# Kernel optimization log

Measured on AMD Instinct MI355X. Metric: run time of the kernel, lower is better.

The kernel has to match this reference:

```python
import jax, jax.numpy as jnp
import numpy as np

N_NODES, N_EDGES, CH, FEAT = 20000, 320000, 256, 118


def setup_inputs() -> dict:
    key = jax.random.key(0)
    ks = jax.random.split(key, 8)
    x = jax.random.uniform(ks[0], (N_NODES, FEAT), dtype=jnp.float32)
    edge_index = jax.random.randint(ks[1], (2, N_EDGES), 0, N_NODES, dtype=jnp.int64)
    s = 0.05
    W_embed = jax.random.normal(ks[2], (FEAT, CH), dtype=jnp.float32) * s
    b_embed = jnp.zeros((CH,), jnp.float32)
    W1 = jax.random.normal(ks[3], (CH, CH), dtype=jnp.float32) * s
    b1 = jnp.zeros((CH,), jnp.float32)
    W2 = jax.random.normal(ks[4], (CH, CH), dtype=jnp.float32) * s
    b2 = jnp.zeros((CH,), jnp.float32)
    return {"x": x, "edge_index": edge_index, "W_embed": W_embed, "b_embed": b_embed,
            "W1": W1, "b1": b1, "W2": W2, "b2": b2}


def reference(x, edge_index, W_embed, b_embed, W1, b1, W2, b2):
    n = x.shape[0]
    # node embedding: Linear(118 -> C)
    h = x @ W_embed + b_embed  # [N, C]
    src, dst = edge_index[0], edge_index[1]
    # message: gather x_j per edge, dense1 + exact GELU (dropout = identity in eval)
    msg = jax.nn.gelu(h[src] @ W1 + b1, approximate=False)  # [E, C]
    # mean aggregation into destination nodes
    agg = jax.ops.segment_sum(msg, dst, num_segments=n)  # [N, C]
    cnt = jax.ops.segment_sum(jnp.ones((msg.shape[0],), msg.dtype), dst, num_segments=n)
    agg = agg / jnp.maximum(cnt, 1.0)[:, None]
    # update: dense2 + exact GELU
    out = jax.nn.gelu(agg @ W2 + b2, approximate=False)  # [N, C]
    # final mean over channel dim
    return out.mean(axis=1)  # [N]
```

## Files before the change

### kernel.cpp

```cpp
#include <hip/hip_runtime.h>
#include <math.h>

#define N_NODES 20000
#define N_EDGES 320000
#define CH      256
#define FEAT    118
#define CAP     48

typedef float    f32x4 __attribute__((ext_vector_type(4)));
typedef short    s16x8 __attribute__((ext_vector_type(8)));
typedef _Float16 f16x4 __attribute__((ext_vector_type(4)));
typedef _Float16 f16x8 __attribute__((ext_vector_type(8)));
typedef unsigned short u16;

union Frag  { s16x8 v; u16 u[8]; };
union FragH { f16x8 v; _Float16 h[8]; };

__device__ __forceinline__ float gelu_exact(float x) {
    return 0.5f * x * (1.0f + erff(x * 0.70710678118654752f));
}
__device__ __forceinline__ u16 f2bf(float f) {
    unsigned u = __float_as_uint(f);
    u = (u + 0x7FFFu + ((u >> 16) & 1u)) >> 16;
    return (u16)u;
}
__device__ __forceinline__ float bf2f(u16 h) { return __uint_as_float(((unsigned)h) << 16); }

__global__ __launch_bounds__(256) void prep(const float* __restrict__ x,
                                            const int* __restrict__ ei,
                                            const float* __restrict__ We,
                                            const float* __restrict__ be,
                                            const float* __restrict__ W1,
                                            const float* __restrict__ b1,
                                            const float* __restrict__ W2,
                                            u16* __restrict__ xh, u16* __restrict__ xl,
                                            int* __restrict__ cnt, int* __restrict__ bins,
                                            _Float16* __restrict__ w2h, _Float16* __restrict__ w2l,
                                            u16* __restrict__ wch, u16* __restrict__ wcl,
                                            float* __restrict__ bc) {
    const int b = blockIdx.x, tid = threadIdx.x;
    if (b < 1250) {
        __shared__ float xs[16][132];
        {
            int r = tid >> 4, ci = tid & 15;
            const float* xrow = x + (size_t)(b * 16 + r) * FEAT;
            #pragma unroll
            for (int it = 0; it < 8; it++) {
                int col = ci + it * 16;
                xs[r][col] = (col < FEAT) ? xrow[col] : 0.0f;
            }
        }
        __syncthreads();
        int lane = tid & 63, ks = tid >> 6;
        int row = lane & 15, k0 = ks * 32 + (lane >> 4) * 8;
        Frag hi, lo;
        #pragma unroll
        for (int j = 0; j < 8; j++) {
            float v = xs[row][k0 + j];
            u16 h = f2bf(v);
            hi.u[j] = h; lo.u[j] = f2bf(v - bf2f(h));
        }
        size_t fid = (size_t)b * 256 + tid;
        ((s16x8*)xh)[fid] = hi.v;
        ((s16x8*)xl)[fid] = lo.v;
    } else if (b < 2500) {
        int e = (b - 1250) * 256 + tid;
        int s = ei[e];
        int d = ei[N_EDGES + e];
        int p = atomicAdd(&cnt[d], 1);
        if (p < CAP) bins[(size_t)d * CAP + p] = s;
    } else if (b < 2532) {
        int fid = (b - 2500) * 256 + tid;
        int lane = fid & 63, ks = (fid >> 6) & 7, nt = fid >> 9;
        int n = nt * 16 + (lane & 15);
        int k0 = ks * 32 + (lane >> 4) * 8;
        FragH hi, lo;
        #pragma unroll
        for (int j = 0; j < 8; j++) {
            float v = W2[(size_t)(k0 + j) * 256 + n];
            _Float16 h = (_Float16)v;
            hi.h[j] = h;
            lo.h[j] = (_Float16)((v - (float)h) * 4096.0f);
        }
        ((f16x8*)w2h)[fid] = hi.v;
        ((f16x8*)w2l)[fid] = lo.v;
    } else {
        int f = b - 2532;
        int n = tid;
        if (f < 128) {
            float acc = 0.0f;
            if (f < FEAT) {
                const float* wr = We + (size_t)f * 256;
                #pragma unroll 8
                for (int c = 0; c < 256; c++) acc += wr[c] * W1[(size_t)c * 256 + n];
            }
            int nt = n >> 4, lm = n & 15, ks = f >> 5, q = (f >> 3) & 3, j = f & 7;
            size_t idx = (((size_t)nt * 4 + ks) * 64 + q * 16 + lm) * 8 + j;
            u16 h = f2bf(acc);
            wch[idx] = h;
            wcl[idx] = f2bf(acc - bf2f(h));
        } else {
            float acc = b1[n];
            #pragma unroll 8
            for (int c = 0; c < 256; c++) acc += be[c] * W1[(size_t)c * 256 + n];
            bc[n] = acc;
        }
    }
}

__global__ __launch_bounds__(256) void gemm_main(const u16* __restrict__ Ah_, const u16* __restrict__ Al_,
                                                 const u16* __restrict__ Bh_, const u16* __restrict__ Bl_,
                                                 const float* __restrict__ bias,
                                                 _Float16* __restrict__ Mout) {
    __shared__ _Float16 Ls[16][256];
    const int tid = threadIdx.x, wave = tid >> 6, lane = tid & 63;
    const int quad = lane >> 4, lm = lane & 15;
    const int mt = blockIdx.x, nt0 = wave * 4;
    const s16x8* Ah = (const s16x8*)Ah_; const s16x8* Al = (const s16x8*)Al_;
    const s16x8* Bh = (const s16x8*)Bh_; const s16x8* Bl = (const s16x8*)Bl_;
    f32x4 acc[4] = {f32x4{0,0,0,0}, f32x4{0,0,0,0}, f32x4{0,0,0,0}, f32x4{0,0,0,0}};
    #pragma unroll
    for (int ks = 0; ks < 4; ks++) {
        s16x8 a_h = Ah[((size_t)mt * 4 + ks) * 64 + lane];
        s16x8 a_l = Al[((size_t)mt * 4 + ks) * 64 + lane];
        #pragma unroll
        for (int t = 0; t < 4; t++) {
            s16x8 bh = Bh[((size_t)(nt0 + t) * 4 + ks) * 64 + lane];
            s16x8 bl = Bl[((size_t)(nt0 + t) * 4 + ks) * 64 + lane];
            acc[t] = __builtin_amdgcn_mfma_f32_16x16x32_bf16(a_h, bh, acc[t], 0, 0, 0);
            acc[t] = __builtin_amdgcn_mfma_f32_16x16x32_bf16(a_l, bh, acc[t], 0, 0, 0);
            acc[t] = __builtin_amdgcn_mfma_f32_16x16x32_bf16(a_h, bl, acc[t], 0, 0, 0);
        }
    }
    #pragma unroll
    for (int t = 0; t < 4; t++) {
        float bn = bias[(nt0 + t) * 16 + lm];
        #pragma unroll
        for (int r = 0; r < 4; r++)
            Ls[quad * 4 + r][(nt0 + t) * 16 + lm] = (_Float16)gelu_exact(acc[t][r] + bn);
    }
    __syncthreads();
    s16x8* dst = (s16x8*)Mout + (size_t)mt * 512;
    const s16x8* src = (const s16x8*)&Ls[0][0];
    dst[tid]       = src[tid];
    dst[256 + tid] = src[256 + tid];
}

__global__ __launch_bounds__(256) void aggregate(const _Float16* __restrict__ M,
                                                 const int* __restrict__ cnt,
                                                 const int* __restrict__ bins,
                                                 _Float16* __restrict__ aggf) {
    int node = (blockIdx.x * 256 + threadIdx.x) >> 6;
    int lane = threadIdx.x & 63;
    int half = lane >> 5, lh = lane & 31;
    int c = cnt[node];
    int cc = min(c, CAP);
    int myid = (lane < cc) ? bins[(size_t)node * CAP + lane] : 0;
    float a[8] = {0.f, 0.f, 0.f, 0.f, 0.f, 0.f, 0.f, 0.f};
    for (int j = 0; j < cc; j += 8) {
        f16x8 v[4];
        #pragma unroll
        for (int u = 0; u < 4; u++) {
            int e = min(j + u * 2 + half, cc - 1);
            int s = __shfl(myid, e, 64);
            v[u] = *(const f16x8*)(M + (size_t)s * CH + lh * 8);
        }
        #pragma unroll
        for (int u = 0; u < 4; u++) {
            if (j + u * 2 + half < cc) {
                #pragma unroll
                for (int q = 0; q < 8; q++) a[q] += (float)v[u][q];
            }
        }
    }
    #pragma unroll
    for (int q = 0; q < 8; q++) a[q] += __shfl_xor(a[q], 32, 64);
    if (half == 0) {
        float inv = 1.0f / (float)max(c, 1);
        FragH o;
        #pragma unroll
        for (int q = 0; q < 8; q++) o.h[q] = (_Float16)(a[q] * inv);
        int mt = node >> 4, lm = node & 15;
        int ks = lh >> 2, quad = lh & 3;
        size_t base = (((size_t)mt * 8 + ks) * 64 + quad * 16 + lm) * 8;
        *(f16x8*)(aggf + base) = o.v;
    }
}

__global__ __launch_bounds__(256) void gemm_mean(const _Float16* __restrict__ Af_,
                                                 const _Float16* __restrict__ Bh_, const _Float16* __restrict__ Bl_,
                                                 const float* __restrict__ bias,
                                                 float* __restrict__ out) {
    __shared__ float part[4][32];
    const int tid = threadIdx.x, wave = tid >> 6, lane = tid & 63;
    const int quad = lane >> 4, lm = lane & 15;
    const int mt0 = blockIdx.x * 2, nt0 = wave * 4;
    const f16x8* Af = (const f16x8*)Af_;
    const f16x8* Bh = (const f16x8*)Bh_; const f16x8* Bl = (const f16x8*)Bl_;
    f32x4 acch[2][4], accl[2][4];
    #pragma unroll
    for (int mi = 0; mi < 2; mi++)
        #pragma unroll
        for (int t = 0; t < 4; t++) {
            acch[mi][t] = f32x4{0.f, 0.f, 0.f, 0.f};
            accl[mi][t] = f32x4{0.f, 0.f, 0.f, 0.f};
        }
    #pragma unroll
    for (int ks = 0; ks < 8; ks++) {
        f16x8 a0 = Af[((size_t)(mt0 + 0) * 8 + ks) * 64 + lane];
        f16x8 a1 = Af[((size_t)(mt0 + 1) * 8 + ks) * 64 + lane];
        #pragma unroll
        for (int t = 0; t < 4; t++) {
            f16x8 bh = Bh[((size_t)(nt0 + t) * 8 + ks) * 64 + lane];
            f16x8 bl = Bl[((size_t)(nt0 + t) * 8 + ks) * 64 + lane];
            acch[0][t] = __builtin_amdgcn_mfma_f32_16x16x32_f16(a0, bh, acch[0][t], 0, 0, 0);
            accl[0][t] = __builtin_amdgcn_mfma_f32_16x16x32_f16(a0, bl, accl[0][t], 0, 0, 0);
            acch[1][t] = __builtin_amdgcn_mfma_f32_16x16x32_f16(a1, bh, acch[1][t], 0, 0, 0);
            accl[1][t] = __builtin_amdgcn_mfma_f32_16x16x32_f16(a1, bl, accl[1][t], 0, 0, 0);
        }
    }
    float p[2][4] = {{0.f,0.f,0.f,0.f},{0.f,0.f,0.f,0.f}};
    #pragma unroll
    for (int t = 0; t < 4; t++) {
        float bn = bias[(nt0 + t) * 16 + lm];
        #pragma unroll
        for (int mi = 0; mi < 2; mi++)
            #pragma unroll
            for (int r = 0; r < 4; r++)
                p[mi][r] += gelu_exact(acch[mi][t][r] + accl[mi][t][r] * (1.0f / 4096.0f) + bn);
    }
    #pragma unroll
    for (int off = 1; off < 16; off <<= 1)
        #pragma unroll
        for (int mi = 0; mi < 2; mi++)
            #pragma unroll
            for (int r = 0; r < 4; r++)
                p[mi][r] += __shfl_xor(p[mi][r], off, 64);
    if (lm == 0)
        #pragma unroll
        for (int mi = 0; mi < 2; mi++)
            #pragma unroll
            for (int r = 0; r < 4; r++)
                part[wave][mi * 16 + quad * 4 + r] = p[mi][r];
    __syncthreads();
    if (tid < 32) {
        float s = part[0][tid] + part[1][tid] + part[2][tid] + part[3][tid];
        out[blockIdx.x * 32 + tid] = s * (1.0f / 256.0f);
    }
}

extern "C" void kernel_launch(void* const* d_in, const int* in_sizes, int n_in,
                              void* d_out, int out_size, void* d_ws, size_t ws_size,
                              hipStream_t stream) {
    const float* x  = (const float*)d_in[0];
    const int*   ei = (const int*)d_in[1];
    const float* We = (const float*)d_in[2];
    const float* be = (const float*)d_in[3];
    const float* W1 = (const float*)d_in[4];
    const float* b1 = (const float*)d_in[5];
    const float* W2 = (const float*)d_in[6];
    const float* b2 = (const float*)d_in[7];
    float* out = (float*)d_out;

    char* ws = (char*)d_ws;
    size_t off = 0;
    u16* xh = (u16*)(ws + off);
    _Float16* aggf = (_Float16*)(ws + off);
    off += 5120000;
    u16* xl = (u16*)(ws + off); off += 5120000;
    _Float16* M = (_Float16*)(ws + off); off += 10240000;
    u16* wch = (u16*)(ws + off); off += 65536;
    u16* wcl = (u16*)(ws + off); off += 65536;
    _Float16* w2h = (_Float16*)(ws + off); off += 131072;
    _Float16* w2l = (_Float16*)(ws + off); off += 131072;
    float* bc = (float*)(ws + off); off += 1024;
    int* cnt  = (int*)(ws + off); off += N_NODES * 4;
    int* bins = (int*)(ws + off); off += (size_t)N_NODES * CAP * 4;

    hipMemsetAsync(cnt, 0, N_NODES * sizeof(int), stream);
    prep<<<2661, 256, 0, stream>>>(x, ei, We, be, W1, b1, W2,
                                   xh, xl, cnt, bins, w2h, w2l, wch, wcl, bc);
    gemm_main<<<N_NODES / 16, 256, 0, stream>>>(xh, xl, wch, wcl, bc, M);
    aggregate<<<N_NODES / 4, 256, 0, stream>>>(M, cnt, bins, aggf);
    gemm_mean<<<N_NODES / 32, 256, 0, stream>>>(aggf, w2h, w2l, b2, out);
}
```

Baseline: 150.8 us.

## Fuse x split into node GEMM, merge aggregation with update GEMM, drop memset

```diff
diff --git a/kernel.cpp b/kernel.cpp
--- a/kernel.cpp
+++ b/kernel.cpp
@@ -26,51 +26,18 @@
 }
 __device__ __forceinline__ float bf2f(u16 h) { return __uint_as_float(((unsigned)h) << 16); }
 
-__global__ __launch_bounds__(256) void prep(const float* __restrict__ x,
-                                            const int* __restrict__ ei,
-                                            const float* __restrict__ We,
-                                            const float* __restrict__ be,
-                                            const float* __restrict__ W1,
-                                            const float* __restrict__ b1,
-                                            const float* __restrict__ W2,
-                                            u16* __restrict__ xh, u16* __restrict__ xl,
-                                            int* __restrict__ cnt, int* __restrict__ bins,
-                                            _Float16* __restrict__ w2h, _Float16* __restrict__ w2l,
-                                            u16* __restrict__ wch, u16* __restrict__ wcl,
-                                            float* __restrict__ bc) {
+__global__ __launch_bounds__(256) void prep0(const float* __restrict__ We,
+                                             const float* __restrict__ be,
+                                             const float* __restrict__ W1,
+                                             const float* __restrict__ b1,
+                                             const float* __restrict__ W2,
+                                             _Float16* __restrict__ w2h, _Float16* __restrict__ w2l,
+                                             u16* __restrict__ wch, u16* __restrict__ wcl,
+                                             float* __restrict__ bc,
+                                             int* __restrict__ cnt) {
     const int b = blockIdx.x, tid = threadIdx.x;
-    if (b < 1250) {
-        __shared__ float xs[16][132];
-        {
-            int r = tid >> 4, ci = tid & 15;
-            const float* xrow = x + (size_t)(b * 16 + r) * FEAT;
-            #pragma unroll
-            for (int it = 0; it < 8; it++) {
-                int col = ci + it * 16;
-                xs[r][col] = (col < FEAT) ? xrow[col] : 0.0f;
-            }
-        }
-        __syncthreads();
-        int lane = tid & 63, ks = tid >> 6;
-        int row = lane & 15, k0 = ks * 32 + (lane >> 4) * 8;
-        Frag hi, lo;
-        #pragma unroll
-        for (int j = 0; j < 8; j++) {
-            float v = xs[row][k0 + j];
-            u16 h = f2bf(v);
-            hi.u[j] = h; lo.u[j] = f2bf(v - bf2f(h));
-        }
-        size_t fid = (size_t)b * 256 + tid;
-        ((s16x8*)xh)[fid] = hi.v;
-        ((s16x8*)xl)[fid] = lo.v;
-    } else if (b < 2500) {
-        int e = (b - 1250) * 256 + tid;
-        int s = ei[e];
-        int d = ei[N_EDGES + e];
-        int p = atomicAdd(&cnt[d], 1);
-        if (p < CAP) bins[(size_t)d * CAP + p] = s;
-    } else if (b < 2532) {
-        int fid = (b - 2500) * 256 + tid;
+    if (b < 32) {
+        int fid = b * 256 + tid;
         int lane = fid & 63, ks = (fid >> 6) & 7, nt = fid >> 9;
         int n = nt * 16 + (lane & 15);
         int k0 = ks * 32 + (lane >> 4) * 8;
@@ -84,8 +51,8 @@
         }
         ((f16x8*)w2h)[fid] = hi.v;
         ((f16x8*)w2l)[fid] = lo.v;
-    } else {
-        int f = b - 2532;
+    } else if (b < 161) {
+        int f = b - 32;
         int n = tid;
         if (f < 128) {
             float acc = 0.0f;
@@ -105,31 +72,65 @@
             for (int c = 0; c < 256; c++) acc += be[c] * W1[(size_t)c * 256 + n];
             bc[n] = acc;
         }
-    }
-}
-
-__global__ __launch_bounds__(256) void gemm_main(const u16* __restrict__ Ah_, const u16* __restrict__ Al_,
-                                                 const u16* __restrict__ Bh_, const u16* __restrict__ Bl_,
-                                                 const float* __restrict__ bias,
-                                                 _Float16* __restrict__ Mout) {
+    } else {
+        int idx = (b - 161) * 256 + tid;
+        if (idx < N_NODES) cnt[idx] = 0;
+    }
+}
+
+__global__ __launch_bounds__(256) void main_fused(const float* __restrict__ x,
+                                                  const int* __restrict__ ei,
+                                                  const u16* __restrict__ Bh_, const u16* __restrict__ Bl_,
+                                                  const float* __restrict__ bias,
+                                                  int* __restrict__ cnt, int* __restrict__ bins,
+                                                  _Float16* __restrict__ Mout) {
+    if (blockIdx.x >= 1250) {
+        int e = (blockIdx.x - 1250) * 256 + threadIdx.x;
+        int s = ei[e];
+        int d = ei[N_EDGES + e];
+        int p = atomicAdd(&cnt[d], 1);
+        if (p < CAP) bins[(size_t)d * CAP + p] = s;
+        return;
+    }
+    __shared__ float xs[16][132];
     __shared__ _Float16 Ls[16][256];
     const int tid = threadIdx.x, wave = tid >> 6, lane = tid & 63;
     const int quad = lane >> 4, lm = lane & 15;
     const int mt = blockIdx.x, nt0 = wave * 4;
-    const s16x8* Ah = (const s16x8*)Ah_; const s16x8* Al = (const s16x8*)Al_;
+    {
+        int r = tid >> 4, ci = tid & 15;
+        const float* xrow = x + (size_t)(mt * 16 + r) * FEAT;
+        #pragma unroll
+        for (int it = 0; it < 8; it++) {
+            int col = ci + it * 16;
+            xs[r][col] = (col < FEAT) ? xrow[col] : 0.0f;
+        }
+    }
+    __syncthreads();
+    s16x8 a_h[4], a_l[4];
+    #pragma unroll
+    for (int ks = 0; ks < 4; ks++) {
+        int k0 = ks * 32 + quad * 8;
+        Frag hi, lo;
+        #pragma unroll
+        for (int j = 0; j < 8; j++) {
+            float v = xs[lm][k0 + j];
+            u16 h = f2bf(v);
+            hi.u[j] = h; lo.u[j] = f2bf(v - bf2f(h));
+        }
+        a_h[ks] = hi.v; a_l[ks] = lo.v;
+    }
     const s16x8* Bh = (const s16x8*)Bh_; const s16x8* Bl = (const s16x8*)Bl_;
     f32x4 acc[4] = {f32x4{0,0,0,0}, f32x4{0,0,0,0}, f32x4{0,0,0,0}, f32x4{0,0,0,0}};
     #pragma unroll
     for (int ks = 0; ks < 4; ks++) {
-        s16x8 a_h = Ah[((size_t)mt * 4 + ks) * 64 + lane];
-        s16x8 a_l = Al[((size_t)mt * 4 + ks) * 64 + lane];
         #pragma unroll
         for (int t = 0; t < 4; t++) {
             s16x8 bh = Bh[((size_t)(nt0 + t) * 4 + ks) * 64 + lane];
             s16x8 bl = Bl[((size_t)(nt0 + t) * 4 + ks) * 64 + lane];
-            acc[t] = __builtin_amdgcn_mfma_f32_16x16x32_bf16(a_h, bh, acc[t], 0, 0, 0);
-            acc[t] = __builtin_amdgcn_mfma_f32_16x16x32_bf16(a_l, bh, acc[t], 0, 0, 0);
-            acc[t] = __builtin_amdgcn_mfma_f32_16x16x32_bf16(a_h, bl, acc[t], 0, 0, 0);
+            acc[t] = __builtin_amdgcn_mfma_f32_16x16x32_bf16(a_h[ks], bh, acc[t], 0, 0, 0);
+            acc[t] = __builtin_amdgcn_mfma_f32_16x16x32_bf16(a_l[ks], bh, acc[t], 0, 0, 0);
+            acc[t] = __builtin_amdgcn_mfma_f32_16x16x32_bf16(a_h[ks], bl, acc[t], 0, 0, 0);
         }
     }
     #pragma unroll
@@ -146,106 +147,89 @@
     dst[256 + tid] = src[256 + tid];
 }
 
-__global__ __launch_bounds__(256) void aggregate(const _Float16* __restrict__ M,
-                                                 const int* __restrict__ cnt,
-                                                 const int* __restrict__ bins,
-                                                 _Float16* __restrict__ aggf) {
-    int node = (blockIdx.x * 256 + threadIdx.x) >> 6;
-    int lane = threadIdx.x & 63;
-    int half = lane >> 5, lh = lane & 31;
-    int c = cnt[node];
-    int cc = min(c, CAP);
-    int myid = (lane < cc) ? bins[(size_t)node * CAP + lane] : 0;
-    float a[8] = {0.f, 0.f, 0.f, 0.f, 0.f, 0.f, 0.f, 0.f};
-    for (int j = 0; j < cc; j += 8) {
-        f16x8 v[4];
-        #pragma unroll
-        for (int u = 0; u < 4; u++) {
-            int e = min(j + u * 2 + half, cc - 1);
-            int s = __shfl(myid, e, 64);
-            v[u] = *(const f16x8*)(M + (size_t)s * CH + lh * 8);
-        }
-        #pragma unroll
-        for (int u = 0; u < 4; u++) {
-            if (j + u * 2 + half < cc) {
-                #pragma unroll
-                for (int q = 0; q < 8; q++) a[q] += (float)v[u][q];
+__global__ __launch_bounds__(256) void aggmean(const _Float16* __restrict__ M,
+                                               const int* __restrict__ cnt,
+                                               const int* __restrict__ bins,
+                                               const _Float16* __restrict__ Bh_,
+                                               const _Float16* __restrict__ Bl_,
+                                               const float* __restrict__ bias,
+                                               float* __restrict__ out) {
+    __shared__ f16x8 af[8][64];
+    __shared__ float part[4][16];
+    const int tid = threadIdx.x, wave = tid >> 6, lane = tid & 63;
+    const int half = lane >> 5, lh = lane & 31;
+    const int node0 = blockIdx.x * 16;
+    for (int ni = 0; ni < 4; ni++) {
+        int node = node0 + wave * 4 + ni;
+        int c = cnt[node];
+        int cc = min(c, CAP);
+        int myid = (lane < cc) ? bins[(size_t)node * CAP + lane] : 0;
+        float a[8] = {0.f, 0.f, 0.f, 0.f, 0.f, 0.f, 0.f, 0.f};
+        for (int j = 0; j < cc; j += 8) {
+            f16x8 v[4];
+            #pragma unroll
+            for (int u = 0; u < 4; u++) {
+                int e = min(j + u * 2 + half, cc - 1);
+                int s = __shfl(myid, e, 64);
+                v[u] = *(const f16x8*)(M + (size_t)s * CH + lh * 8);
             }
-        }
-    }
-    #pragma unroll
-    for (int q = 0; q < 8; q++) a[q] += __shfl_xor(a[q], 32, 64);
-    if (half == 0) {
-        float inv = 1.0f / (float)max(c, 1);
-        FragH o;
-        #pragma unroll
-        for (int q = 0; q < 8; q++) o.h[q] = (_Float16)(a[q] * inv);
-        int mt = node >> 4, lm = node & 15;
-        int ks = lh >> 2, quad = lh & 3;
-        size_t base = (((size_t)mt * 8 + ks) * 64 + quad * 16 + lm) * 8;
-        *(f16x8*)(aggf + base) = o.v;
-    }
-}
-
-__global__ __launch_bounds__(256) void gemm_mean(const _Float16* __restrict__ Af_,
-                                                 const _Float16* __restrict__ Bh_, const _Float16* __restrict__ Bl_,
-                                                 const float* __restrict__ bias,
-                                                 float* __restrict__ out) {
-    __shared__ float part[4][32];
-    const int tid = threadIdx.x, wave = tid >> 6, lane = tid & 63;
+            #pragma unroll
+            for (int u = 0; u < 4; u++) {
+                if (j + u * 2 + half < cc) {
+                    #pragma unroll
+                    for (int q = 0; q < 8; q++) a[q] += (float)v[u][q];
+                }
+            }
+        }
+        #pragma unroll
+        for (int q = 0; q < 8; q++) a[q] += __shfl_xor(a[q], 32, 64);
+        if (half == 0) {
+            float inv = 1.0f / (float)max(c, 1);
+            FragH o;
+            #pragma unroll
+            for (int q = 0; q < 8; q++) o.h[q] = (_Float16)(a[q] * inv);
+            af[lh >> 2][(lh & 3) * 16 + (wave * 4 + ni)] = o.v;
+        }
+    }
+    __syncthreads();
     const int quad = lane >> 4, lm = lane & 15;
-    const int mt0 = blockIdx.x * 2, nt0 = wave * 4;
-    const f16x8* Af = (const f16x8*)Af_;
-    const f16x8* Bh = (const f16x8*)Bh_; const f16x8* Bl = (const f16x8*)Bl_;
-    f32x4 acch[2][4], accl[2][4];
-    #pragma unroll
-    for (int mi = 0; mi < 2; mi++)
-        #pragma unroll
-        for (int t = 0; t < 4; t++) {
-            acch[mi][t] = f32x4{0.f, 0.f, 0.f, 0.f};
-            accl[mi][t] = f32x4{0.f, 0.f, 0.f, 0.f};
-        }
+    const int nt0 = wave * 4;
+    const f16x8* Bh = (const f16x8*)Bh_;
+    const f16x8* Bl = (const f16x8*)Bl_;
+    f32x4 acch[4] = {f32x4{0,0,0,0}, f32x4{0,0,0,0}, f32x4{0,0,0,0}, f32x4{0,0,0,0}};
+    f32x4 accl[4] = {f32x4{0,0,0,0}, f32x4{0,0,0,0}, f32x4{0,0,0,0}, f32x4{0,0,0,0}};
     #pragma unroll
     for (int ks = 0; ks < 8; ks++) {
-        f16x8 a0 = Af[((size_t)(mt0 + 0) * 8 + ks) * 64 + lane];
-        f16x8 a1 = Af[((size_t)(mt0 + 1) * 8 + ks) * 64 + lane];
+        f16x8 a = af[ks][lane];
         #pragma unroll
         for (int t = 0; t < 4; t++) {
             f16x8 bh = Bh[((size_t)(nt0 + t) * 8 + ks) * 64 + lane];
             f16x8 bl = Bl[((size_t)(nt0 + t) * 8 + ks) * 64 + lane];
-            acch[0][t] = __builtin_amdgcn_mfma_f32_16x16x32_f16(a0, bh, acch[0][t], 0, 0, 0);
-            accl[0][t] = __builtin_amdgcn_mfma_f32_16x16x32_f16(a0, bl, accl[0][t], 0, 0, 0);
-            acch[1][t] = __builtin_amdgcn_mfma_f32_16x16x32_f16(a1, bh, acch[1][t], 0, 0, 0);
-            accl[1][t] = __builtin_amdgcn_mfma_f32_16x16x32_f16(a1, bl, accl[1][t], 0, 0, 0);
-        }
-    }
-    float p[2][4] = {{0.f,0.f,0.f,0.f},{0.f,0.f,0.f,0.f}};
+            acch[t] = __builtin_amdgcn_mfma_f32_16x16x32_f16(a, bh, acch[t], 0, 0, 0);
+            accl[t] = __builtin_amdgcn_mfma_f32_16x16x32_f16(a, bl, accl[t], 0, 0, 0);
+        }
+    }
+    float p[4] = {0.f, 0.f, 0.f, 0.f};
     #pragma unroll
     for (int t = 0; t < 4; t++) {
         float bn = bias[(nt0 + t) * 16 + lm];
         #pragma unroll
-        for (int mi = 0; mi < 2; mi++)
-            #pragma unroll
-            for (int r = 0; r < 4; r++)
-                p[mi][r] += gelu_exact(acch[mi][t][r] + accl[mi][t][r] * (1.0f / 4096.0f) + bn);
+        for (int r = 0; r < 4; r++)
+            p[r] += gelu_exact(acch[t][r] + accl[t][r] * (1.0f / 4096.0f) + bn);
     }
     #pragma unroll
     for (int off = 1; off < 16; off <<= 1)
         #pragma unroll
-        for (int mi = 0; mi < 2; mi++)
-            #pragma unroll
-            for (int r = 0; r < 4; r++)
-                p[mi][r] += __shfl_xor(p[mi][r], off, 64);
+        for (int r = 0; r < 4; r++)
+            p[r] += __shfl_xor(p[r], off, 64);
     if (lm == 0)
         #pragma unroll
-        for (int mi = 0; mi < 2; mi++)
-            #pragma unroll
-            for (int r = 0; r < 4; r++)
-                part[wave][mi * 16 + quad * 4 + r] = p[mi][r];
-    __syncthreads();
-    if (tid < 32) {
+        for (int r = 0; r < 4; r++)
+            part[wave][quad * 4 + r] = p[r];
+    __syncthreads();
+    if (tid < 16) {
         float s = part[0][tid] + part[1][tid] + part[2][tid] + part[3][tid];
-        out[blockIdx.x * 32 + tid] = s * (1.0f / 256.0f);
+        out[node0 + tid] = s * (1.0f / 256.0f);
     }
 }
 
@@ -264,10 +248,6 @@
 
     char* ws = (char*)d_ws;
     size_t off = 0;
-    u16* xh = (u16*)(ws + off);
-    _Float16* aggf = (_Float16*)(ws + off);
-    off += 5120000;
-    u16* xl = (u16*)(ws + off); off += 5120000;
     _Float16* M = (_Float16*)(ws + off); off += 10240000;
     u16* wch = (u16*)(ws + off); off += 65536;
     u16* wcl = (u16*)(ws + off); off += 65536;
@@ -277,10 +257,7 @@
     int* cnt  = (int*)(ws + off); off += N_NODES * 4;
     int* bins = (int*)(ws + off); off += (size_t)N_NODES * CAP * 4;
 
-    hipMemsetAsync(cnt, 0, N_NODES * sizeof(int), stream);
-    prep<<<2661, 256, 0, stream>>>(x, ei, We, be, W1, b1, W2,
-                                   xh, xl, cnt, bins, w2h, w2l, wch, wcl, bc);
-    gemm_main<<<N_NODES / 16, 256, 0, stream>>>(xh, xl, wch, wcl, bc, M);
-    aggregate<<<N_NODES / 4, 256, 0, stream>>>(M, cnt, bins, aggf);
-    gemm_mean<<<N_NODES / 32, 256, 0, stream>>>(aggf, w2h, w2l, b2, out);
-}
+    prep0<<<240, 256, 0, stream>>>(We, be, W1, b1, W2, w2h, w2l, wch, wcl, bc, cnt);
+    main_fused<<<2500, 256, 0, stream>>>(x, ei, wch, wcl, bc, cnt, bins, M);
+    aggmean<<<N_NODES / 16, 256, 0, stream>>>(M, cnt, bins, w2h, w2l, b2, out);
+}
```

Result: slower. 156.4 us (+3.7%).

## Fuse x bf16 split into embedding GEMM, fold memset into prep, widen gather unroll

Applied to the files above, without the earlier changes.

```diff
diff --git a/kernel.cpp b/kernel.cpp
--- a/kernel.cpp
+++ b/kernel.cpp
@@ -26,51 +26,18 @@
 }
 __device__ __forceinline__ float bf2f(u16 h) { return __uint_as_float(((unsigned)h) << 16); }
 
-__global__ __launch_bounds__(256) void prep(const float* __restrict__ x,
-                                            const int* __restrict__ ei,
-                                            const float* __restrict__ We,
-                                            const float* __restrict__ be,
-                                            const float* __restrict__ W1,
-                                            const float* __restrict__ b1,
-                                            const float* __restrict__ W2,
-                                            u16* __restrict__ xh, u16* __restrict__ xl,
-                                            int* __restrict__ cnt, int* __restrict__ bins,
-                                            _Float16* __restrict__ w2h, _Float16* __restrict__ w2l,
-                                            u16* __restrict__ wch, u16* __restrict__ wcl,
-                                            float* __restrict__ bc) {
+__global__ __launch_bounds__(256) void prep0(const float* __restrict__ We,
+                                             const float* __restrict__ be,
+                                             const float* __restrict__ W1,
+                                             const float* __restrict__ b1,
+                                             const float* __restrict__ W2,
+                                             _Float16* __restrict__ w2h, _Float16* __restrict__ w2l,
+                                             u16* __restrict__ wch, u16* __restrict__ wcl,
+                                             float* __restrict__ bc,
+                                             int* __restrict__ cnt) {
     const int b = blockIdx.x, tid = threadIdx.x;
-    if (b < 1250) {
-        __shared__ float xs[16][132];
-        {
-            int r = tid >> 4, ci = tid & 15;
-            const float* xrow = x + (size_t)(b * 16 + r) * FEAT;
-            #pragma unroll
-            for (int it = 0; it < 8; it++) {
-                int col = ci + it * 16;
-                xs[r][col] = (col < FEAT) ? xrow[col] : 0.0f;
-            }
-        }
-        __syncthreads();
-        int lane = tid & 63, ks = tid >> 6;
-        int row = lane & 15, k0 = ks * 32 + (lane >> 4) * 8;
-        Frag hi, lo;
-        #pragma unroll
-        for (int j = 0; j < 8; j++) {
-            float v = xs[row][k0 + j];
-            u16 h = f2bf(v);
-            hi.u[j] = h; lo.u[j] = f2bf(v - bf2f(h));
-        }
-        size_t fid = (size_t)b * 256 + tid;
-        ((s16x8*)xh)[fid] = hi.v;
-        ((s16x8*)xl)[fid] = lo.v;
-    } else if (b < 2500) {
-        int e = (b - 1250) * 256 + tid;
-        int s = ei[e];
-        int d = ei[N_EDGES + e];
-        int p = atomicAdd(&cnt[d], 1);
-        if (p < CAP) bins[(size_t)d * CAP + p] = s;
-    } else if (b < 2532) {
-        int fid = (b - 2500) * 256 + tid;
+    if (b < 32) {
+        int fid = b * 256 + tid;
         int lane = fid & 63, ks = (fid >> 6) & 7, nt = fid >> 9;
         int n = nt * 16 + (lane & 15);
         int k0 = ks * 32 + (lane >> 4) * 8;
@@ -84,8 +51,8 @@
         }
         ((f16x8*)w2h)[fid] = hi.v;
         ((f16x8*)w2l)[fid] = lo.v;
-    } else {
-        int f = b - 2532;
+    } else if (b < 161) {
+        int f = b - 32;
         int n = tid;
         if (f < 128) {
             float acc = 0.0f;
@@ -105,31 +72,65 @@
             for (int c = 0; c < 256; c++) acc += be[c] * W1[(size_t)c * 256 + n];
             bc[n] = acc;
         }
-    }
-}
-
-__global__ __launch_bounds__(256) void gemm_main(const u16* __restrict__ Ah_, const u16* __restrict__ Al_,
-                                                 const u16* __restrict__ Bh_, const u16* __restrict__ Bl_,
-                                                 const float* __restrict__ bias,
-                                                 _Float16* __restrict__ Mout) {
+    } else {
+        int idx = (b - 161) * 256 + tid;
+        if (idx < N_NODES) cnt[idx] = 0;
+    }
+}
+
+__global__ __launch_bounds__(256) void main_fused(const float* __restrict__ x,
+                                                  const int* __restrict__ ei,
+                                                  const u16* __restrict__ Bh_, const u16* __restrict__ Bl_,
+                                                  const float* __restrict__ bias,
+                                                  int* __restrict__ cnt, int* __restrict__ bins,
+                                                  _Float16* __restrict__ Mout) {
+    if (blockIdx.x >= 1250) {
+        int e = (blockIdx.x - 1250) * 256 + threadIdx.x;
+        int s = ei[e];
+        int d = ei[N_EDGES + e];
+        int p = atomicAdd(&cnt[d], 1);
+        if (p < CAP) bins[(size_t)d * CAP + p] = s;
+        return;
+    }
+    __shared__ float xs[16][132];
     __shared__ _Float16 Ls[16][256];
     const int tid = threadIdx.x, wave = tid >> 6, lane = tid & 63;
     const int quad = lane >> 4, lm = lane & 15;
     const int mt = blockIdx.x, nt0 = wave * 4;
-    const s16x8* Ah = (const s16x8*)Ah_; const s16x8* Al = (const s16x8*)Al_;
+    {
+        int r = tid >> 4, ci = tid & 15;
+        const float* xrow = x + (size_t)(mt * 16 + r) * FEAT;
+        #pragma unroll
+        for (int it = 0; it < 8; it++) {
+            int col = ci + it * 16;
+            xs[r][col] = (col < FEAT) ? xrow[col] : 0.0f;
+        }
+    }
+    __syncthreads();
+    s16x8 a_h[4], a_l[4];
+    #pragma unroll
+    for (int ks = 0; ks < 4; ks++) {
+        int k0 = ks * 32 + quad * 8;
+        Frag hi, lo;
+        #pragma unroll
+        for (int j = 0; j < 8; j++) {
+            float v = xs[lm][k0 + j];
+            u16 h = f2bf(v);
+            hi.u[j] = h; lo.u[j] = f2bf(v - bf2f(h));
+        }
+        a_h[ks] = hi.v; a_l[ks] = lo.v;
+    }
     const s16x8* Bh = (const s16x8*)Bh_; const s16x8* Bl = (const s16x8*)Bl_;
     f32x4 acc[4] = {f32x4{0,0,0,0}, f32x4{0,0,0,0}, f32x4{0,0,0,0}, f32x4{0,0,0,0}};
     #pragma unroll
     for (int ks = 0; ks < 4; ks++) {
-        s16x8 a_h = Ah[((size_t)mt * 4 + ks) * 64 + lane];
-        s16x8 a_l = Al[((size_t)mt * 4 + ks) * 64 + lane];
         #pragma unroll
         for (int t = 0; t < 4; t++) {
             s16x8 bh = Bh[((size_t)(nt0 + t) * 4 + ks) * 64 + lane];
             s16x8 bl = Bl[((size_t)(nt0 + t) * 4 + ks) * 64 + lane];
-            acc[t] = __builtin_amdgcn_mfma_f32_16x16x32_bf16(a_h, bh, acc[t], 0, 0, 0);
-            acc[t] = __builtin_amdgcn_mfma_f32_16x16x32_bf16(a_l, bh, acc[t], 0, 0, 0);
-            acc[t] = __builtin_amdgcn_mfma_f32_16x16x32_bf16(a_h, bl, acc[t], 0, 0, 0);
+            acc[t] = __builtin_amdgcn_mfma_f32_16x16x32_bf16(a_h[ks], bh, acc[t], 0, 0, 0);
+            acc[t] = __builtin_amdgcn_mfma_f32_16x16x32_bf16(a_l[ks], bh, acc[t], 0, 0, 0);
+            acc[t] = __builtin_amdgcn_mfma_f32_16x16x32_bf16(a_h[ks], bl, acc[t], 0, 0, 0);
         }
     }
     #pragma unroll
@@ -157,16 +158,16 @@
     int cc = min(c, CAP);
     int myid = (lane < cc) ? bins[(size_t)node * CAP + lane] : 0;
     float a[8] = {0.f, 0.f, 0.f, 0.f, 0.f, 0.f, 0.f, 0.f};
-    for (int j = 0; j < cc; j += 8) {
-        f16x8 v[4];
-        #pragma unroll
-        for (int u = 0; u < 4; u++) {
+    for (int j = 0; j < cc; j += 16) {
+        f16x8 v[8];
+        #pragma unroll
+        for (int u = 0; u < 8; u++) {
             int e = min(j + u * 2 + half, cc - 1);
             int s = __shfl(myid, e, 64);
             v[u] = *(const f16x8*)(M + (size_t)s * CH + lh * 8);
         }
         #pragma unroll
-        for (int u = 0; u < 4; u++) {
+        for (int u = 0; u < 8; u++) {
             if (j + u * 2 + half < cc) {
                 #pragma unroll
                 for (int q = 0; q < 8; q++) a[q] += (float)v[u][q];
@@ -264,11 +265,8 @@
 
     char* ws = (char*)d_ws;
     size_t off = 0;
-    u16* xh = (u16*)(ws + off);
-    _Float16* aggf = (_Float16*)(ws + off);
-    off += 5120000;
-    u16* xl = (u16*)(ws + off); off += 5120000;
     _Float16* M = (_Float16*)(ws + off); off += 10240000;
+    _Float16* aggf = (_Float16*)(ws + off); off += 10240000;
     u16* wch = (u16*)(ws + off); off += 65536;
     u16* wcl = (u16*)(ws + off); off += 65536;
     _Float16* w2h = (_Float16*)(ws + off); off += 131072;
@@ -277,10 +275,8 @@
     int* cnt  = (int*)(ws + off); off += N_NODES * 4;
     int* bins = (int*)(ws + off); off += (size_t)N_NODES * CAP * 4;
 
-    hipMemsetAsync(cnt, 0, N_NODES * sizeof(int), stream);
-    prep<<<2661, 256, 0, stream>>>(x, ei, We, be, W1, b1, W2,
-                                   xh, xl, cnt, bins, w2h, w2l, wch, wcl, bc);
-    gemm_main<<<N_NODES / 16, 256, 0, stream>>>(xh, xl, wch, wcl, bc, M);
+    prep0<<<240, 256, 0, stream>>>(We, be, W1, b1, W2, w2h, w2l, wch, wcl, bc, cnt);
+    main_fused<<<2500, 256, 0, stream>>>(x, ei, wch, wcl, bc, cnt, bins, M);
     aggregate<<<N_NODES / 4, 256, 0, stream>>>(M, cnt, bins, aggf);
     gemm_mean<<<N_NODES / 32, 256, 0, stream>>>(aggf, w2h, w2l, b2, out);
 }
```

Result: no change. 150.5 us (-0.2%).
